# Kernel tuning notes

Measured on AMD Instinct MI355X. Metric: run time of the kernel, lower is better.

## Reference

```python
import jax, jax.numpy as jnp
import numpy as np

WIN = 8          # window side
N = WIN * WIN    # tokens per window = 64
C = 180          # channels
H = 6            # heads
D = C // H       # head dim = 30


def _relative_index():
    coords = jnp.stack(jnp.meshgrid(jnp.arange(WIN), jnp.arange(WIN), indexing='ij'))
    coords = coords.reshape(2, -1)                       # (2, N)
    rel = coords[:, :, None] - coords[:, None, :]        # (2, N, N)
    idx = (rel[0] + WIN - 1) * (2 * WIN - 1) + (rel[1] + WIN - 1)
    return idx.reshape(-1)                               # (N*N,) int


def setup_inputs() -> dict:
    key = jax.random.key(0)
    ks = jax.random.split(key, 6)
    B, WNum = 4096, 1024
    windows = jax.random.normal(ks[0], (B, N, C), dtype=jnp.float32)
    mask = jax.random.normal(ks[1], (WNum, N, N), dtype=jnp.float32)
    w_qkv = jax.random.normal(ks[2], (C, 3 * C), dtype=jnp.float32) * 0.02
    bias_table = jax.random.normal(ks[3], ((2 * WIN - 1) ** 2, H), dtype=jnp.float32) * 0.02
    w_proj = jax.random.normal(ks[4], (C, C), dtype=jnp.float32) * 0.02
    b_proj = jnp.zeros((C,), dtype=jnp.float32)
    return {"windows": windows, "mask": mask, "w_qkv": w_qkv,
            "bias_table": bias_table, "w_proj": w_proj, "b_proj": b_proj}


def reference(windows, mask, w_qkv, bias_table, w_proj, b_proj):
    B, n, c = windows.shape
    WNum = mask.shape[0]
    rel_idx = _relative_index()

    # qkv projection: (B, N, 3C) -> (3, B, H, N, D)
    qkv = (windows @ w_qkv).reshape(B, n, 3, H, D).transpose(2, 0, 3, 1, 4)
    q, k, v = qkv[0], qkv[1], qkv[2]

    scale = 1.0 / jnp.sqrt(jnp.float32(D))
    scores = jnp.einsum('bhnd,bhmd->bhnm', q, k) * scale     # (B, H, N, N)

    # relative position bias gather: (N*N, H) -> (H, N, N)
    rel_bias = bias_table[rel_idx].reshape(n, n, H).transpose(2, 0, 1)
    scores = scores + rel_bias[None]

    # per-window mask add
    scores = scores.reshape(B // WNum, WNum, H, n, n) + mask[None, :, None, :, :]
    scores = scores.reshape(B, H, n, n)

    attn = jax.nn.softmax(scores, axis=-1)
    out = jnp.einsum('bhnm,bhmd->bhnd', attn, v)             # (B, H, N, D)
    z = out.transpose(0, 2, 1, 3).reshape(B, n, c)
    return z @ w_proj + b_proj
```

## Files before the change

### kernel.cpp

```cpp
#include <hip/hip_runtime.h>


typedef __bf16 bf16;
typedef bf16 bf16x8 __attribute__((ext_vector_type(8)));
typedef float f32x4 __attribute__((ext_vector_type(4)));

#define MFMA(a, b, c) __builtin_amdgcn_mfma_f32_16x16x32_bf16(a, b, c, 0, 0, 0)

__global__ void prep_kernel(const float* __restrict__ wqkv,
                            const float* __restrict__ wproj,
                            const float* __restrict__ btab,
                            bf16* __restrict__ wqkvT,
                            bf16* __restrict__ wprojT,
                            float* __restrict__ relb)
{
    const int idx = blockIdx.x * 256 + threadIdx.x;
    if (idx < 110592) {
        const int oc = idx / 192, kk = idx - oc * 192;
        const int h = oc / 96, r = oc - h * 96;
        const int sec = r >> 5, d = r & 31;
        wqkvT[idx] = (bf16)((kk < 180 && d < 30) ? wqkv[kk * 540 + sec * 180 + h * 30 + d] : 0.f);
    } else if (idx < 147456) {
        const int r = idx - 110592;
        const int n = r / 192, k = r - n * 192;
        wprojT[r] = (bf16)((n < 180 && k < 180) ? wproj[k * 180 + n] : 0.f);
    } else if (idx < 172032) {
        const int r = idx - 147456;
        const int h = r >> 12;
        const int ij = r & 4095;
        const int i = ij >> 6, j = ij & 63;
        const int rel = ((i >> 3) - (j >> 3) + 7) * 15 + ((i & 7) - (j & 7) + 7);
        relb[r] = btab[rel * 6 + h];
    }
}

__global__ __launch_bounds__(384, 4)
void swin_mfma(const float* __restrict__ xg_all,
               const float* __restrict__ mask_all,
               const float* __restrict__ bproj,
               const bf16* __restrict__ wqkvT,
               const bf16* __restrict__ wprojT,
               const float* __restrict__ relb,
               float* __restrict__ outg)
{
    __shared__ __align__(16) short xb[64 * 200];

    const int b    = blockIdx.x;
    const int tid  = threadIdx.x;
    const int w    = tid >> 6;
    const int lane = tid & 63;
    const int l15  = lane & 15;
    const int g    = lane >> 4;

    const float* xg    = xg_all + (size_t)b * 11520;
    const float* maskw = mask_all + (size_t)(b & 1023) * 4096;

    for (int e = tid; e < 640; e += 384) {
        const int i = e / 10;
        ((unsigned*)(xb + i * 200 + 180))[e - i * 10] = 0u;
    }
    for (int e = tid; e < 5760; e += 384) {
        const int i = e / 90;
        const int c = 2 * e - i * 180;
        const float2 v = *reinterpret_cast<const float2*>(xg + 2 * e);
        const unsigned lo = (unsigned)__builtin_bit_cast(unsigned short, (bf16)v.x);
        const unsigned hi = (unsigned)__builtin_bit_cast(unsigned short, (bf16)v.y);
        *reinterpret_cast<unsigned*>(xb + i * 200 + c) = lo | (hi << 16);
    }
    __syncthreads();

    const bf16* wqh = wqkvT + (size_t)(w * 96) * 192;
    const int rowoff = l15 * 192 + 8 * g;

    bf16x8 qf[4];
    {
        f32x4 aq[2][4];
        #pragma unroll
        for (int ct = 0; ct < 2; ct++)
            #pragma unroll
            for (int tt = 0; tt < 4; tt++) aq[ct][tt] = (f32x4)0.f;
        for (int ks = 0; ks < 6; ks++) {
            bf16x8 xf[4];
            #pragma unroll
            for (int tt = 0; tt < 4; tt++)
                xf[tt] = *reinterpret_cast<const bf16x8*>(xb + (16 * tt + l15) * 200 + 32 * ks + 8 * g);
            #pragma unroll
            for (int ct = 0; ct < 2; ct++) {
                const bf16x8 wf = *reinterpret_cast<const bf16x8*>(wqh + ct * 16 * 192 + rowoff + 32 * ks);
                #pragma unroll
                for (int tt = 0; tt < 4; tt++)
                    aq[ct][tt] = MFMA(wf, xf[tt], aq[ct][tt]);
            }
        }
        #pragma unroll
        for (int tt = 0; tt < 4; tt++)
            #pragma unroll
            for (int s = 0; s < 8; s++)
                qf[tt][s] = (bf16)(aq[s >> 2][tt][s & 3] * 0.18257418583505537f);
    }
    __builtin_amdgcn_sched_barrier(0);

    bf16x8 kf[4];
    {
        f32x4 ak[2][4];
        #pragma unroll
        for (int ct = 0; ct < 2; ct++)
            #pragma unroll
            for (int tt = 0; tt < 4; tt++) ak[ct][tt] = (f32x4)0.f;
        for (int ks = 0; ks < 6; ks++) {
            bf16x8 xf[4];
            #pragma unroll
            for (int tt = 0; tt < 4; tt++)
                xf[tt] = *reinterpret_cast<const bf16x8*>(xb + (16 * tt + l15) * 200 + 32 * ks + 8 * g);
            #pragma unroll
            for (int ct = 0; ct < 2; ct++) {
                const bf16x8 wf = *reinterpret_cast<const bf16x8*>(wqh + (2 + ct) * 16 * 192 + rowoff + 32 * ks);
                #pragma unroll
                for (int tt = 0; tt < 4; tt++)
                    ak[ct][tt] = MFMA(wf, xf[tt], ak[ct][tt]);
            }
        }
        #pragma unroll
        for (int tt = 0; tt < 4; tt++)
            #pragma unroll
            for (int s = 0; s < 8; s++)
                kf[tt][s] = (bf16)(ak[s >> 2][tt][s & 3]);
    }
    __builtin_amdgcn_sched_barrier(0);

    bf16x8 pf[4][2];
    {
        const float* relh = relb + w * 4096;
        #pragma unroll
        for (int it = 0; it < 4; it++) {
            f32x4 stj[4];
            #pragma unroll
            for (int jt = 0; jt < 4; jt++) stj[jt] = MFMA(kf[jt], qf[it], (f32x4)0.f);

            const int i = 16 * it + l15;
            const float* rbb = relh + i * 64 + 4 * g;
            const float* mkb = maskw + i * 64 + 4 * g;
            float mx = -1e30f;
            #pragma unroll
            for (int jt = 0; jt < 4; jt++) {
                const float4 rb = *reinterpret_cast<const float4*>(rbb + 16 * jt);
                const float4 mk = *reinterpret_cast<const float4*>(mkb + 16 * jt);
                stj[jt][0] += rb.x + mk.x;
                stj[jt][1] += rb.y + mk.y;
                stj[jt][2] += rb.z + mk.z;
                stj[jt][3] += rb.w + mk.w;
                #pragma unroll
                for (int r = 0; r < 4; r++) mx = fmaxf(mx, stj[jt][r]);
            }
            mx = fmaxf(mx, __shfl_xor(mx, 16));
            mx = fmaxf(mx, __shfl_xor(mx, 32));
            float sum = 0.f;
            #pragma unroll
            for (int jt = 0; jt < 4; jt++)
                #pragma unroll
                for (int r = 0; r < 4; r++) {
                    const float e = __expf(stj[jt][r] - mx);
                    stj[jt][r] = e;
                    sum += e;
                }
            sum += __shfl_xor(sum, 16);
            sum += __shfl_xor(sum, 32);
            const float inv = 1.0f / sum;
            #pragma unroll
            for (int k2 = 0; k2 < 2; k2++)
                #pragma unroll
                for (int s = 0; s < 8; s++)
                    pf[it][k2][s] = (bf16)(stj[2 * k2 + (s >> 2)][s & 3] * inv);
        }
    }
    __builtin_amdgcn_sched_barrier(0);

    bf16x8 vf[2][2];
    {
        f32x4 av[4][2];
        #pragma unroll
        for (int tt = 0; tt < 4; tt++) { av[tt][0] = (f32x4)0.f; av[tt][1] = (f32x4)0.f; }
        for (int ks = 0; ks < 6; ks++) {
            bf16x8 xf[4];
            #pragma unroll
            for (int tt = 0; tt < 4; tt++)
                xf[tt] = *reinterpret_cast<const bf16x8*>(xb + (16 * tt + l15) * 200 + 32 * ks + 8 * g);
            #pragma unroll
            for (int cv = 0; cv < 2; cv++) {
                const bf16x8 wf = *reinterpret_cast<const bf16x8*>(wqh + (4 + cv) * 16 * 192 + rowoff + 32 * ks);
                #pragma unroll
                for (int tt = 0; tt < 4; tt++)
                    av[tt][cv] = MFMA(xf[tt], wf, av[tt][cv]);
            }
        }
        #pragma unroll
        for (int cv = 0; cv < 2; cv++)
            #pragma unroll
            for (int k2 = 0; k2 < 2; k2++)
                #pragma unroll
                for (int s = 0; s < 8; s++)
                    vf[cv][k2][s] = (bf16)(av[2 * k2 + (s >> 2)][cv][s & 3]);
    }
    __builtin_amdgcn_sched_barrier(0);

    f32x4 zacc[4][2];
    #pragma unroll
    for (int it = 0; it < 4; it++) { zacc[it][0] = (f32x4)0.f; zacc[it][1] = (f32x4)0.f; }
    #pragma unroll
    for (int k2 = 0; k2 < 2; k2++)
        #pragma unroll
        for (int cv = 0; cv < 2; cv++)
            #pragma unroll
            for (int it = 0; it < 4; it++)
                zacc[it][cv] = MFMA(pf[it][k2], vf[cv][k2], zacc[it][cv]);

    __syncthreads();
    #pragma unroll
    for (int cv = 0; cv < 2; cv++) {
        const int d = 16 * cv + l15;
        if (d < 30) {
            #pragma unroll
            for (int it = 0; it < 4; it++)
                #pragma unroll
                for (int r = 0; r < 4; r++)
                    xb[(16 * it + 4 * g + r) * 200 + w * 30 + d] =
                        __builtin_bit_cast(short, (bf16)zacc[it][cv][r]);
        }
    }
    __syncthreads();

    f32x4 pa[4][2];
    #pragma unroll
    for (int mt = 0; mt < 4; mt++) { pa[mt][0] = (f32x4)0.f; pa[mt][1] = (f32x4)0.f; }
    for (int ks = 0; ks < 6; ks++) {
        bf16x8 zf[4];
        #pragma unroll
        for (int mt = 0; mt < 4; mt++)
            zf[mt] = *reinterpret_cast<const bf16x8*>(xb + (16 * mt + l15) * 200 + 32 * ks + 8 * g);
        #pragma unroll
        for (int q2 = 0; q2 < 2; q2++) {
            const bf16x8 wf = *reinterpret_cast<const bf16x8*>(
                wprojT + ((2 * w + q2) * 16 + l15) * 192 + 32 * ks + 8 * g);
            #pragma unroll
            for (int mt = 0; mt < 4; mt++)
                pa[mt][q2] = MFMA(zf[mt], wf, pa[mt][q2]);
        }
    }
    #pragma unroll
    for (int q2 = 0; q2 < 2; q2++) {
        const int n = (2 * w + q2) * 16 + l15;
        if (n < 180) {
            const float bn = bproj[n];
            float* const ob = outg + (size_t)b * 11520 + n;
            #pragma unroll
            for (int mt = 0; mt < 4; mt++)
                #pragma unroll
                for (int r = 0; r < 4; r++)
                    ob[(16 * mt + 4 * g + r) * 180] = pa[mt][q2][r] + bn;
        }
    }
}

extern "C" void kernel_launch(void* const* d_in, const int* in_sizes, int n_in,
                              void* d_out, int out_size, void* d_ws, size_t ws_size,
                              hipStream_t stream) {
    const float* windows = (const float*)d_in[0];
    const float* mask    = (const float*)d_in[1];
    const float* wqkv    = (const float*)d_in[2];
    const float* btab    = (const float*)d_in[3];
    const float* wproj   = (const float*)d_in[4];
    const float* bproj   = (const float*)d_in[5];

    bf16*  wqkvT  = (bf16*)d_ws;
    bf16*  wprojT = (bf16*)((char*)d_ws + 221184);
    float* relb   = (float*)((char*)d_ws + 294912);

    hipLaunchKernelGGL(prep_kernel, dim3(672), dim3(256), 0, stream,
                       wqkv, wproj, btab, wqkvT, wprojT, relb);
    hipLaunchKernelGGL(swin_mfma, dim3(4096), dim3(384), 0, stream,
                       windows, mask, bproj, wqkvT, wprojT, relb, (float*)d_out);
}
```

Before: 341.6 us.

## Split attention into per-head-pair blocks with separate projection kernel and bf16 x prepass

Breaks the fused one-block-per-window kernel into three stages. A prepass converts x to bf16 in MFMA fragment order, if the workspace is large enough. An attention kernel then runs 128-thread blocks that each handle two heads, and writes bf16 head outputs into the output buffer as scratch. A separate projection kernel reloads those outputs through LDS and applies w_proj. The goal is more, smaller blocks without LDS, for better occupancy and latency hiding, at the cost of extra launches and extra global round trips for x and z.

```diff
diff --git a/kernel.cpp b/kernel.cpp
--- a/kernel.cpp
+++ b/kernel.cpp
@@ -7,12 +7,12 @@
 
 #define MFMA(a, b, c) __builtin_amdgcn_mfma_f32_16x16x32_bf16(a, b, c, 0, 0, 0)
 
-__global__ void prep_kernel(const float* __restrict__ wqkv,
-                            const float* __restrict__ wproj,
-                            const float* __restrict__ btab,
-                            bf16* __restrict__ wqkvT,
-                            bf16* __restrict__ wprojT,
-                            float* __restrict__ relb)
+__global__ void prep_w(const float* __restrict__ wqkv,
+                       const float* __restrict__ wproj,
+                       const float* __restrict__ btab,
+                       bf16* __restrict__ wqkvT,
+                       bf16* __restrict__ wprojT,
+                       float* __restrict__ relb)
 {
     const int idx = blockIdx.x * 256 + threadIdx.x;
     if (idx < 110592) {
@@ -34,43 +34,79 @@
     }
 }
 
-__global__ __launch_bounds__(384, 4)
-void swin_mfma(const float* __restrict__ xg_all,
+__global__ __launch_bounds__(256) void prep_x(const float* __restrict__ xg_all,
+                                              bf16* __restrict__ xbf)
+{
+    const int b = blockIdx.x;
+    const float* xg = xg_all + (size_t)b * 11520;
+    bf16* dst = xbf + (size_t)b * 12288;
+    for (int e = threadIdx.x; e < 1536; e += 256) {
+        const int lane = e & 63;
+        const int tt = (e >> 6) & 3;
+        const int ks = e >> 8;
+        const int l15 = lane & 15, g = lane >> 4;
+        const int row = 16 * tt + l15;
+        const int c0 = 32 * ks + 8 * g;
+        bf16x8 v;
+        #pragma unroll
+        for (int s = 0; s < 8; s++) {
+            const int c = c0 + s;
+            v[s] = (bf16)((c < 180) ? xg[row * 180 + c] : 0.f);
+        }
+        *reinterpret_cast<bf16x8*>(dst + (size_t)e * 8) = v;
+    }
+}
+
+template <int XBF>
+__device__ __forceinline__ bf16x8 load_xfrag(const float* __restrict__ xg,
+                                             const bf16* __restrict__ xw,
+                                             int ks, int tt, int l15, int g, int lane)
+{
+    if (XBF) {
+        return *reinterpret_cast<const bf16x8*>(xw + ks * 2048 + tt * 512 + lane * 8);
+    } else {
+        const int row = 16 * tt + l15;
+        const int c0 = 32 * ks + 8 * g;
+        bf16x8 v;
+        if (c0 + 7 < 180) {
+            const float4 a0 = *reinterpret_cast<const float4*>(xg + row * 180 + c0);
+            const float4 a1 = *reinterpret_cast<const float4*>(xg + row * 180 + c0 + 4);
+            v[0] = (bf16)a0.x; v[1] = (bf16)a0.y; v[2] = (bf16)a0.z; v[3] = (bf16)a0.w;
+            v[4] = (bf16)a1.x; v[5] = (bf16)a1.y; v[6] = (bf16)a1.z; v[7] = (bf16)a1.w;
+        } else {
+            #pragma unroll
+            for (int s = 0; s < 8; s++) {
+                const int c = c0 + s;
+                v[s] = (bf16)((c < 180) ? xg[row * 180 + c] : 0.f);
+            }
+        }
+        return v;
+    }
+}
+
+template <int XBF>
+__global__ __launch_bounds__(128, 4)
+void swin_attn(const float* __restrict__ xg_all,
                const float* __restrict__ mask_all,
-               const float* __restrict__ bproj,
                const bf16* __restrict__ wqkvT,
-               const bf16* __restrict__ wprojT,
                const float* __restrict__ relb,
+               const bf16* __restrict__ xbf,
                float* __restrict__ outg)
 {
-    __shared__ __align__(16) short xb[64 * 200];
-
-    const int b    = blockIdx.x;
     const int tid  = threadIdx.x;
-    const int w    = tid >> 6;
     const int lane = tid & 63;
     const int l15  = lane & 15;
     const int g    = lane >> 4;
+    const int bb   = blockIdx.x;
+    const int b    = bb / 3;
+    const int hp   = bb - 3 * b;
+    const int h    = 2 * hp + (tid >> 6);
 
     const float* xg    = xg_all + (size_t)b * 11520;
+    const bf16*  xw    = xbf + (size_t)b * 12288;
     const float* maskw = mask_all + (size_t)(b & 1023) * 4096;
-
-    for (int e = tid; e < 640; e += 384) {
-        const int i = e / 10;
-        ((unsigned*)(xb + i * 200 + 180))[e - i * 10] = 0u;
-    }
-    for (int e = tid; e < 5760; e += 384) {
-        const int i = e / 90;
-        const int c = 2 * e - i * 180;
-        const float2 v = *reinterpret_cast<const float2*>(xg + 2 * e);
-        const unsigned lo = (unsigned)__builtin_bit_cast(unsigned short, (bf16)v.x);
-        const unsigned hi = (unsigned)__builtin_bit_cast(unsigned short, (bf16)v.y);
-        *reinterpret_cast<unsigned*>(xb + i * 200 + c) = lo | (hi << 16);
-    }
-    __syncthreads();
-
-    const bf16* wqh = wqkvT + (size_t)(w * 96) * 192;
-    const int rowoff = l15 * 192 + 8 * g;
+    const bf16*  wqh   = wqkvT + h * 18432;
+    const int rowoff   = l15 * 192 + 8 * g;
 
     bf16x8 qf[4];
     {
@@ -82,14 +118,12 @@
         for (int ks = 0; ks < 6; ks++) {
             bf16x8 xf[4];
             #pragma unroll
-            for (int tt = 0; tt < 4; tt++)
-                xf[tt] = *reinterpret_cast<const bf16x8*>(xb + (16 * tt + l15) * 200 + 32 * ks + 8 * g);
+            for (int tt = 0; tt < 4; tt++) xf[tt] = load_xfrag<XBF>(xg, xw, ks, tt, l15, g, lane);
             #pragma unroll
             for (int ct = 0; ct < 2; ct++) {
-                const bf16x8 wf = *reinterpret_cast<const bf16x8*>(wqh + ct * 16 * 192 + rowoff + 32 * ks);
-                #pragma unroll
-                for (int tt = 0; tt < 4; tt++)
-                    aq[ct][tt] = MFMA(wf, xf[tt], aq[ct][tt]);
+                const bf16x8 wf = *reinterpret_cast<const bf16x8*>(wqh + ct * 3072 + rowoff + 32 * ks);
+                #pragma unroll
+                for (int tt = 0; tt < 4; tt++) aq[ct][tt] = MFMA(wf, xf[tt], aq[ct][tt]);
             }
         }
         #pragma unroll
@@ -110,14 +144,12 @@
         for (int ks = 0; ks < 6; ks++) {
             bf16x8 xf[4];
             #pragma unroll
-            for (int tt = 0; tt < 4; tt++)
-                xf[tt] = *reinterpret_cast<const bf16x8*>(xb + (16 * tt + l15) * 200 + 32 * ks + 8 * g);
+            for (int tt = 0; tt < 4; tt++) xf[tt] = load_xfrag<XBF>(xg, xw, ks, tt, l15, g, lane);
             #pragma unroll
             for (int ct = 0; ct < 2; ct++) {
-                const bf16x8 wf = *reinterpret_cast<const bf16x8*>(wqh + (2 + ct) * 16 * 192 + rowoff + 32 * ks);
-                #pragma unroll
-                for (int tt = 0; tt < 4; tt++)
-                    ak[ct][tt] = MFMA(wf, xf[tt], ak[ct][tt]);
+                const bf16x8 wf = *reinterpret_cast<const bf16x8*>(wqh + (2 + ct) * 3072 + rowoff + 32 * ks);
+                #pragma unroll
+                for (int tt = 0; tt < 4; tt++) ak[ct][tt] = MFMA(wf, xf[tt], ak[ct][tt]);
             }
         }
         #pragma unroll
@@ -130,7 +162,7 @@
 
     bf16x8 pf[4][2];
     {
-        const float* relh = relb + w * 4096;
+        const float* relh = relb + h * 4096;
         #pragma unroll
         for (int it = 0; it < 4; it++) {
             f32x4 stj[4];
@@ -183,14 +215,12 @@
         for (int ks = 0; ks < 6; ks++) {
             bf16x8 xf[4];
             #pragma unroll
-            for (int tt = 0; tt < 4; tt++)
-                xf[tt] = *reinterpret_cast<const bf16x8*>(xb + (16 * tt + l15) * 200 + 32 * ks + 8 * g);
+            for (int tt = 0; tt < 4; tt++) xf[tt] = load_xfrag<XBF>(xg, xw, ks, tt, l15, g, lane);
             #pragma unroll
             for (int cv = 0; cv < 2; cv++) {
-                const bf16x8 wf = *reinterpret_cast<const bf16x8*>(wqh + (4 + cv) * 16 * 192 + rowoff + 32 * ks);
-                #pragma unroll
-                for (int tt = 0; tt < 4; tt++)
-                    av[tt][cv] = MFMA(xf[tt], wf, av[tt][cv]);
+                const bf16x8 wf = *reinterpret_cast<const bf16x8*>(wqh + (4 + cv) * 3072 + rowoff + 32 * ks);
+                #pragma unroll
+                for (int tt = 0; tt < 4; tt++) av[tt][cv] = MFMA(xf[tt], wf, av[tt][cv]);
             }
         }
         #pragma unroll
@@ -214,7 +244,7 @@
             for (int it = 0; it < 4; it++)
                 zacc[it][cv] = MFMA(pf[it][k2], vf[cv][k2], zacc[it][cv]);
 
-    __syncthreads();
+    bf16* zb = (bf16*)(outg + (size_t)b * 11520);
     #pragma unroll
     for (int cv = 0; cv < 2; cv++) {
         const int d = 16 * cv + l15;
@@ -223,32 +253,68 @@
             for (int it = 0; it < 4; it++)
                 #pragma unroll
                 for (int r = 0; r < 4; r++)
-                    xb[(16 * it + 4 * g + r) * 200 + w * 30 + d] =
-                        __builtin_bit_cast(short, (bf16)zacc[it][cv][r]);
+                    zb[(16 * it + 4 * g + r) * 192 + h * 30 + d] = (bf16)zacc[it][cv][r];
+        }
+    }
+}
+
+__global__ __launch_bounds__(256, 4)
+void proj_kernel(const bf16* __restrict__ wprojT,
+                 const float* __restrict__ bproj,
+                 float* __restrict__ outg)
+{
+    __shared__ __align__(16) short zs[64 * 200];
+    const int b    = blockIdx.x;
+    const int tid  = threadIdx.x;
+    const int w2   = tid >> 6;
+    const int lane = tid & 63;
+    const int l15  = lane & 15;
+    const int g    = lane >> 4;
+
+    const bf16* zsrc = (const bf16*)(outg + (size_t)b * 11520);
+    for (int e = tid; e < 1600; e += 256) {
+        const int row = e / 25;
+        const int sl  = e - row * 25;
+        short* const zrow = zs + row * 200;
+        if (sl < 22) {
+            *reinterpret_cast<uint4*>(zrow + sl * 8) =
+                *reinterpret_cast<const uint4*>(zsrc + row * 192 + sl * 8);
+        } else if (sl == 22) {
+            *reinterpret_cast<uint2*>(zrow + 176) =
+                *reinterpret_cast<const uint2*>(zsrc + row * 192 + 176);
+            *reinterpret_cast<uint2*>(zrow + 180) = make_uint2(0u, 0u);
+        } else if (sl == 23) {
+            *reinterpret_cast<uint4*>(zrow + 184) = make_uint4(0u, 0u, 0u, 0u);
+        } else {
+            *reinterpret_cast<uint4*>(zrow + 192) = make_uint4(0u, 0u, 0u, 0u);
         }
     }
     __syncthreads();
 
-    f32x4 pa[4][2];
-    #pragma unroll
-    for (int mt = 0; mt < 4; mt++) { pa[mt][0] = (f32x4)0.f; pa[mt][1] = (f32x4)0.f; }
+    f32x4 pa[4][3];
+    #pragma unroll
+    for (int mt = 0; mt < 4; mt++)
+        #pragma unroll
+        for (int q3 = 0; q3 < 3; q3++) pa[mt][q3] = (f32x4)0.f;
+
     for (int ks = 0; ks < 6; ks++) {
         bf16x8 zf[4];
         #pragma unroll
         for (int mt = 0; mt < 4; mt++)
-            zf[mt] = *reinterpret_cast<const bf16x8*>(xb + (16 * mt + l15) * 200 + 32 * ks + 8 * g);
-        #pragma unroll
-        for (int q2 = 0; q2 < 2; q2++) {
+            zf[mt] = *reinterpret_cast<const bf16x8*>(zs + (16 * mt + l15) * 200 + 32 * ks + 8 * g);
+        #pragma unroll
+        for (int q3 = 0; q3 < 3; q3++) {
+            const int nt = 3 * w2 + q3;
             const bf16x8 wf = *reinterpret_cast<const bf16x8*>(
-                wprojT + ((2 * w + q2) * 16 + l15) * 192 + 32 * ks + 8 * g);
+                wprojT + (nt * 16 + l15) * 192 + 32 * ks + 8 * g);
             #pragma unroll
             for (int mt = 0; mt < 4; mt++)
-                pa[mt][q2] = MFMA(zf[mt], wf, pa[mt][q2]);
-        }
-    }
-    #pragma unroll
-    for (int q2 = 0; q2 < 2; q2++) {
-        const int n = (2 * w + q2) * 16 + l15;
+                pa[mt][q3] = MFMA(zf[mt], wf, pa[mt][q3]);
+        }
+    }
+    #pragma unroll
+    for (int q3 = 0; q3 < 3; q3++) {
+        const int n = (3 * w2 + q3) * 16 + l15;
         if (n < 180) {
             const float bn = bproj[n];
             float* const ob = outg + (size_t)b * 11520 + n;
@@ -256,7 +322,7 @@
             for (int mt = 0; mt < 4; mt++)
                 #pragma unroll
                 for (int r = 0; r < 4; r++)
-                    ob[(16 * mt + 4 * g + r) * 180] = pa[mt][q2][r] + bn;
+                    ob[(16 * mt + 4 * g + r) * 180] = pa[mt][q3][r] + bn;
         }
     }
 }
@@ -274,9 +340,20 @@
     bf16*  wqkvT  = (bf16*)d_ws;
     bf16*  wprojT = (bf16*)((char*)d_ws + 221184);
     float* relb   = (float*)((char*)d_ws + 294912);
-
-    hipLaunchKernelGGL(prep_kernel, dim3(672), dim3(256), 0, stream,
+    bf16*  xbf    = (bf16*)((char*)d_ws + 393216);
+
+    const bool use_xbf = ws_size >= (size_t)393216 + (size_t)4096 * 12288 * 2;
+
+    hipLaunchKernelGGL(prep_w, dim3(672), dim3(256), 0, stream,
                        wqkv, wproj, btab, wqkvT, wprojT, relb);
-    hipLaunchKernelGGL(swin_mfma, dim3(4096), dim3(384), 0, stream,
-                       windows, mask, bproj, wqkvT, wprojT, relb, (float*)d_out);
-}
+    if (use_xbf) {
+        hipLaunchKernelGGL(prep_x, dim3(4096), dim3(256), 0, stream, windows, xbf);
+        hipLaunchKernelGGL(swin_attn<1>, dim3(12288), dim3(128), 0, stream,
+                           windows, mask, wqkvT, relb, xbf, (float*)d_out);
+    } else {
+        hipLaunchKernelGGL(swin_attn<0>, dim3(12288), dim3(128), 0, stream,
+                           windows, mask, wqkvT, relb, xbf, (float*)d_out);
+    }
+    hipLaunchKernelGGL(proj_kernel, dim3(4096), dim3(256), 0, stream,
+                       wprojT, bproj, (float*)d_out);
+}
```

Result: slower. 545.2 us (+59.6%).
